# Performance work log

Hardware: AMD Instinct MI355X
Metric: run time of the kernel (lower is better)

## Reference

```python
import jax, jax.numpy as jnp
import numpy as np

B, T, N, F = 8, 24, 207, 16
H = 64            # hidden_dim
DH = 16           # dims_hyper[-1] / node-embedding out
DA = 4 * F        # temporal attention dim_out
DS = 64           # ss_gal gcn out dim (last_ss_gal_dim)
GDEP = 2
ALPHA, BETA, GAMMA = 0.05, 0.95, 0.95
TA = 2.0


def _lin(x, w, b=None):
    y = x @ w
    return y if b is None else y + b


def gcn_hyper(x, A, W, b):
    # x: [B,N,C], A: [N,N] static. h <- a*x + g * einsum('nvc,vw->nwc', h, A)
    h = x
    outs = [h]
    for _ in range(GDEP):
        h = ALPHA * x + GAMMA * jnp.einsum('bvc,vw->bwc', h, A)
        outs.append(h)
    return _lin(jnp.concatenate(outs, axis=-1), W, b)


def gcn_gru(x, A_dyn, A_sta, W, b):
    # x: [B,N,C], A_dyn: [B,N,N], A_sta: [N,N]
    h = x
    outs = [h]
    for _ in range(GDEP):
        h = (ALPHA * x
             + BETA * jnp.einsum('bvw,bvc->bwc', A_dyn, h)     # bmm(A^T, h)
             + GAMMA * jnp.einsum('bvc,vw->bwc', h, A_sta))
        outs.append(h)
    return _lin(jnp.concatenate(outs, axis=-1), W, b)


def gcn_ssgal(x, A, W, b):
    # x: [B*,N,C], A: [B*,N,N]
    h = x
    outs = [h]
    for _ in range(GDEP):
        h = ALPHA * x + GAMMA * jnp.einsum('bvw,bvc->bwc', A, h)
        outs.append(h)
    return _lin(jnp.concatenate(outs, axis=-1), W, b)


def setup_inputs() -> dict:
    key = jax.random.key(0)
    ks = jax.random.split(key, 32)
    i = iter(range(32))
    w = lambda *s: (0.02 * jax.random.normal(ks[next(i)], s, dtype=jnp.float32))
    inp = {
        'input_sequence': jax.random.normal(ks[next(i)], (B, T, N, F), dtype=jnp.float32),
        'static_adj': jax.random.uniform(ks[next(i)], (N, N), dtype=jnp.float32),
        # hyper graph generators: mlp in = (GDEP+1)*H -> DH
        'src_gen_w': w((GDEP + 1) * H, DH), 'src_gen_b': w(DH),
        'tgt_gen_w': w((GDEP + 1) * H, DH), 'tgt_gen_b': w(DH),
        # node embeddings: F -> DH
        'src_emb_w': w(F, DH), 'src_emb_b': w(DH),
        'tgt_emb_w': w(F, DH), 'tgt_emb_b': w(DH),
        # GRU gate GCNs: mlp in = (GDEP+1)*(F+H) -> H
        'gru_z_w': w((GDEP + 1) * (F + H), H), 'gru_z_b': w(H),
        'gru_r_w': w((GDEP + 1) * (F + H), H), 'gru_r_b': w(H),
        'gru_c_w': w((GDEP + 1) * (F + H), H), 'gru_c_b': w(H),
        # temporal attention: F -> DA, score DA -> 1
        'attn_q_w': w(F, DA),
        'attn_k_w': w(F, DA), 'attn_k_b': w(DA),
        'attn_s_w': w(DA, 1),
        # ss_gal spatial gcn: (GDEP+1)*F -> DS
        'sgcn_w': w((GDEP + 1) * F, DS), 'sgcn_b': w(DS),
        # predictors
        'short_w': w(DS, F), 'short_b': w(F),
        'long_w': w(H, F), 'long_b': w(F),
        'fus_w': w(DS + H, F), 'fus_b': w(F),
    }
    return inp


def _forward(input_sequence, static_adj,
             src_gen_w, src_gen_b, tgt_gen_w, tgt_gen_b,
             src_emb_w, src_emb_b, tgt_emb_w, tgt_emb_b,
             gru_z_w, gru_z_b, gru_r_w, gru_r_b, gru_c_w, gru_c_b,
             attn_q_w, attn_k_w, attn_k_b, attn_s_w,
             sgcn_w, sgcn_b,
             short_w, short_b, long_w, long_b, fus_w, fus_b):
    batch, steps, nodes = input_sequence.shape[0], input_sequence.shape[1], input_sequence.shape[2]
    eye = jnp.eye(nodes, dtype=input_sequence.dtype)

    def cell(x_t, h):
        # x_t: [B,N,F], h: [B,N,H]
        src_ctx = gcn_hyper(h, static_adj, src_gen_w, src_gen_b)   # [B,N,DH]
        tgt_ctx = gcn_hyper(h, static_adj, tgt_gen_w, tgt_gen_b)
        s = jnp.tanh(TA * _lin(x_t, src_emb_w, src_emb_b) * src_ctx)
        t = jnp.tanh(TA * _lin(x_t, tgt_emb_w, tgt_emb_b) * tgt_ctx)
        asym = jnp.einsum('bnc,bmc->bnm', s, t) - jnp.einsum('bnc,bmc->bnm', t, s)
        adj = jax.nn.relu(jnp.tanh(TA * asym)) + eye
        adj = adj / (adj.sum(axis=-1, keepdims=True) + 1e-8)
        gi = jnp.concatenate([x_t, h], axis=-1)
        z = jax.nn.sigmoid(gcn_gru(gi, adj, static_adj, gru_z_w, gru_z_b))
        r = jax.nn.sigmoid(gcn_gru(gi, adj, static_adj, gru_r_w, gru_r_b))
        ri = jnp.concatenate([x_t, r * h], axis=-1)
        c = jnp.tanh(gcn_gru(ri, adj, static_adj, gru_c_w, gru_c_b))
        return z * h + (1.0 - z) * c

    h = jnp.zeros((batch, nodes, H), dtype=input_sequence.dtype)
    for t_step in range(0, max(1, steps - 4), 4):
        h = cell(input_sequence[:, t_step], h)

    # ss_gal branch on the last 4 steps
    recent = input_sequence[:, -4:]            # [B,4,N,F]
    target = input_sequence[:, -1]             # [B,N,F]
    # temporal attention
    q = target @ attn_q_w                      # [B,N,DA]
    k = recent @ attn_k_w + attn_k_b           # [B,4,N,DA]
    scores = jnp.tanh(q[:, None, :, None, :] + k[:, :, None, :, :])  # [B,4,N,N,DA]
    scores = jnp.squeeze(scores @ attn_s_w, axis=-1)                  # [B,4,N,N]
    attn = jax.nn.softmax(scores, axis=-1)
    dyn_adj = static_adj[None] + attn.reshape(-1, nodes, nodes)       # [B*4,N,N]
    rh = recent.reshape(-1, nodes, recent.shape[-1])                  # [B*4,N,F]
    rh = gcn_ssgal(rh, dyn_adj, sgcn_w, sgcn_b)                       # [B*4,N,DS]
    rh = jax.nn.relu(rh.reshape(batch, -1, nodes, rh.shape[-1]))      # [B,4,N,DS]
    target = jnp.sum(rh, axis=1)                                       # [B,N,DS]

    short = _lin(target, short_w, short_b)      # [B,N,F]
    h = cell(short, h)                          # final GRU step on short-term prediction
    long = _lin(h, long_w, long_b)              # [B,N,F]
    fused = _lin(jnp.concatenate([target, h], axis=-1), fus_w, fus_b)  # [B,N,F]
    return jnp.stack([short, long, fused], axis=0)  # [3,B,N,F]


def reference(input_sequence, static_adj,
              src_gen_w, src_gen_b, tgt_gen_w, tgt_gen_b,
              src_emb_w, src_emb_b, tgt_emb_w, tgt_emb_b,
              gru_z_w, gru_z_b, gru_r_w, gru_r_b, gru_c_w, gru_c_b,
              attn_q_w, attn_k_w, attn_k_b, attn_s_w,
              sgcn_w, sgcn_b,
              short_w, short_b, long_w, long_b, fus_w, fus_b):
    return _forward(input_sequence, static_adj,
                    src_gen_w, src_gen_b, tgt_gen_w, tgt_gen_b,
                    src_emb_w, src_emb_b, tgt_emb_w, tgt_emb_b,
                    gru_z_w, gru_z_b, gru_r_w, gru_r_b, gru_c_w, gru_c_b,
                    attn_q_w, attn_k_w, attn_k_b, attn_s_w,
                    sgcn_w, sgcn_b,
                    short_w, short_b, long_w, long_b, fus_w, fus_b)
```

## Files before the change

kernel.cpp:

```cpp
#include <hip/hip_runtime.h>


constexpr int B = 8, T = 24, N = 207, F = 16, H = 64, DH = 16;
constexpr int PS = 208;
constexpr float ALPHA = 0.05f, BETA = 0.95f, GAMMA = 0.95f, TA = 2.0f;
constexpr int NF = N * F;
constexpr int BNF = B * N * F;

__device__ __forceinline__ float tanh_fast(float x) { float e = __expf(2.f * x); return 1.f - 2.f / (e + 1.f); }
__device__ __forceinline__ float sigm(float x) { return 1.f / (1.f + __expf(-x)); }
__device__ __forceinline__ float tanh_pade(float x) {
    float x2 = x * x;
    float p = x * (27.f + x2);
    float q = 27.f + 9.f * x2;
    float r = p * __builtin_amdgcn_rcpf(q);
    return fminf(1.f, fmaxf(-1.f, r));
}

__global__ __launch_bounds__(256) void k_build_Ts(const float* __restrict__ adj, float* __restrict__ Ts) {
    int i = blockIdx.x * 256 + threadIdx.x;
    if (i >= N * N) return;
    int w = i / N, v = i % N;
    Ts[(size_t)w * PS + v] = adj[v * N + w];
}

__global__ __launch_bounds__(256) void k_mm_sq(const float* __restrict__ Ain, float* __restrict__ Aout) {
    int bb = blockIdx.z;
    const float* A = Ain + (size_t)bb * PS * PS;
    float* O = Aout + (size_t)bb * PS * PS;
    int w0 = blockIdx.x * 32, v0b = blockIdx.y * 32;
    int tid = threadIdx.x;
    __shared__ float sA[2][32][33], sB[2][32][33];
    float acc[4] = {0, 0, 0, 0};
    int i0 = tid >> 5, j = tid & 31;
    int r = tid >> 3, c4 = (tid & 7) * 4;
    float4 av, bv;
    auto loadT = [&](int u0) {
        av = make_float4(0, 0, 0, 0); bv = make_float4(0, 0, 0, 0);
        int w = w0 + r, u = u0 + r;
        if (w < N) av = *(const float4*)&A[(size_t)w * PS + u0 + c4];
        if (u < N) bv = *(const float4*)&A[(size_t)u * PS + v0b + c4];
    };
    loadT(0);
    int cur = 0;
    for (int t = 0; t < 7; t++) {
        __syncthreads();
        sA[cur][r][c4] = av.x; sA[cur][r][c4 + 1] = av.y; sA[cur][r][c4 + 2] = av.z; sA[cur][r][c4 + 3] = av.w;
        sB[cur][r][c4] = bv.x; sB[cur][r][c4 + 1] = bv.y; sB[cur][r][c4 + 2] = bv.z; sB[cur][r][c4 + 3] = bv.w;
        if (t < 6) loadT((t + 1) * 32);
        __syncthreads();
#pragma unroll 8
        for (int u_ = 0; u_ < 32; u_++) {
            float bvv = sB[cur][u_][j];
#pragma unroll
            for (int k = 0; k < 4; k++) acc[k] += sA[cur][i0 + k * 8][u_] * bvv;
        }
        cur ^= 1;
    }
#pragma unroll
    for (int k = 0; k < 4; k++) {
        int w = w0 + i0 + k * 8, v = v0b + j;
        if (w < N && v < N) O[(size_t)w * PS + v] = acc[k];
    }
}

__global__ __launch_bounds__(256) void k_cell_a(
    const float* __restrict__ h, const float* __restrict__ Ts, const float* __restrict__ A2,
    const float* __restrict__ xseq, int tsel, const float* __restrict__ xbuf,
    const float* __restrict__ Wsrc, const float* __restrict__ bsrc,
    const float* __restrict__ Wtgt, const float* __restrict__ btgt,
    const float* __restrict__ Wes, const float* __restrict__ bes,
    const float* __restrict__ Wet, const float* __restrict__ bet,
    float* __restrict__ s_out, float* __restrict__ t_out, float* __restrict__ catg) {
    int b = blockIdx.y, w0 = blockIdx.x * 16;
    int tid = threadIdx.x, ty = tid >> 4, tx = tid & 15;
    __shared__ float sTs[2][16][33], sA2[2][16][33];
    __shared__ float sH[2][32][64];
    __shared__ float cat[16][193];
    __shared__ float sW[192][16];
    __shared__ float sX[16][16], sWe[16][16];
    float au[4] = {0, 0, 0, 0}, aw[4] = {0, 0, 0, 0};
    const float* hb = h + b * N * H;
    const float* xp = (tsel >= 0) ? (xseq + ((size_t)(b * T + tsel)) * NF) : (xbuf + (size_t)b * NF);
    int pidx = tid & 127;
    int pr = pidx >> 3, pc4 = (pidx & 7) * 4;
    float4 t4;
    float4 h4[2];
    int hr[2], hc[2];
#pragma unroll
    for (int k = 0; k < 2; k++) { int l4 = tid + k * 256; hr[k] = l4 >> 4; hc[k] = (l4 & 15) * 4; }
    auto loadT = [&](int v0) {
        t4 = make_float4(0, 0, 0, 0);
        const float* src = (tid < 128) ? Ts : A2;
        int w = w0 + pr;
        if (w < N) t4 = *(const float4*)&src[(size_t)w * PS + v0 + pc4];
#pragma unroll
        for (int k = 0; k < 2; k++) {
            float4 hv = make_float4(0, 0, 0, 0);
            int v = v0 + hr[k];
            if (v < N) hv = *(const float4*)&hb[(size_t)v * H + hc[k]];
            h4[k] = hv;
        }
    };
    loadT(0);
    int cur = 0;
    for (int t = 0; t < 7; t++) {
        __syncthreads();
        {
            float (*dst)[33] = (tid < 128) ? sTs[cur] : sA2[cur];
            dst[pr][pc4] = t4.x; dst[pr][pc4 + 1] = t4.y; dst[pr][pc4 + 2] = t4.z; dst[pr][pc4 + 3] = t4.w;
        }
#pragma unroll
        for (int k = 0; k < 2; k++) *(float4*)&sH[cur][hr[k]][hc[k]] = h4[k];
        if (t < 6) loadT((t + 1) * 32);
        __syncthreads();
#pragma unroll 8
        for (int v = 0; v < 32; v++) {
            float pu = sTs[cur][ty][v], pw = sA2[cur][ty][v];
#pragma unroll
            for (int j = 0; j < 4; j++) {
                float x = sH[cur][v][tx * 4 + j];
                au[j] += pu * x; aw[j] += pw * x;
            }
        }
        cur ^= 1;
    }
    int w = w0 + ty;
    bool valid = w < N;
    __syncthreads();
    if (valid) {
#pragma unroll
        for (int j = 0; j < 4; j++) {
            int c = tx * 4 + j;
            float hv = hb[w * H + c];
            float u = au[j], w2 = aw[j];
            cat[ty][c] = hv;
            cat[ty][64 + c] = ALPHA * hv + GAMMA * u;
            cat[ty][128 + c] = ALPHA * hv + ALPHA * GAMMA * u + GAMMA * GAMMA * w2;
        }
    } else {
#pragma unroll
        for (int j = 0; j < 4; j++) {
            int c = tx * 4 + j;
            cat[ty][c] = 0; cat[ty][64 + c] = 0; cat[ty][128 + c] = 0;
        }
    }
    {
        float4 wv[3];
#pragma unroll
        for (int k = 0; k < 3; k++) {
            int l4 = tid + k * 256;
            wv[k] = *(const float4*)&Wsrc[l4 * 4];
        }
        float4 xv = make_float4(0, 0, 0, 0), ev = make_float4(0, 0, 0, 0);
        int sr = 0, sc = 0;
        if (tid < 64) {
            sr = tid >> 2; sc = (tid & 3) * 4;
            int n = w0 + sr;
            if (n < N) xv = *(const float4*)&xp[(size_t)n * F + sc];
            ev = *(const float4*)&Wes[tid * 4];
        }
#pragma unroll
        for (int k = 0; k < 3; k++) {
            int l4 = tid + k * 256;
            int r = l4 >> 2, c4 = (l4 & 3) * 4;
            *(float4*)&sW[r][c4] = wv[k];
        }
        if (tid < 64) {
            *(float4*)&sX[sr][sc] = xv;
            *(float4*)&sWe[sr][sc] = ev;
        }
    }
    __syncthreads();
    if (valid) {
#pragma unroll
        for (int j = 0; j < 5; j++) {
            int c = tx * 5 + j;
            float v = (c < 16) ? sX[ty][c] : hb[w * H + (c - 16)];
            catg[((size_t)(b * N + w)) * 240 + c] = v;
        }
    }
    {
        float ctx = bsrc[tx];
#pragma unroll 8
        for (int c = 0; c < 192; c++) ctx += cat[ty][c] * sW[c][tx];
        float xe = bes[tx];
#pragma unroll
        for (int f = 0; f < 16; f++) xe += sX[ty][f] * sWe[f][tx];
        if (valid) s_out[(b * N + w) * DH + tx] = tanh_fast(TA * xe * ctx);
    }
    __syncthreads();
    {
        float4 wv[3];
#pragma unroll
        for (int k = 0; k < 3; k++) {
            int l4 = tid + k * 256;
            wv[k] = *(const float4*)&Wtgt[l4 * 4];
        }
        float4 ev = make_float4(0, 0, 0, 0);
        if (tid < 64) ev = *(const float4*)&Wet[tid * 4];
#pragma unroll
        for (int k = 0; k < 3; k++) {
            int l4 = tid + k * 256;
            int r = l4 >> 2, c4 = (l4 & 3) * 4;
            *(float4*)&sW[r][c4] = wv[k];
        }
        if (tid < 64) *(float4*)&sWe[tid >> 2][(tid & 3) * 4] = ev;
    }
    __syncthreads();
    {
        float ctx = btgt[tx];
#pragma unroll 8
        for (int c = 0; c < 192; c++) ctx += cat[ty][c] * sW[c][tx];
        float xe = bet[tx];
#pragma unroll
        for (int f = 0; f < 16; f++) xe += sX[ty][f] * sWe[f][tx];
        if (valid) t_out[(b * N + w) * DH + tx] = tanh_fast(TA * xe * ctx);
    }
}

__global__ __launch_bounds__(256) void k_cell_bP(const float* __restrict__ s_in, const float* __restrict__ t_in,
                                                 const float* __restrict__ adj, float* __restrict__ P) {
    int b = blockIdx.y, v0 = blockIdx.x * 16;
    int tid = threadIdx.x, ty = tid >> 4, tx = tid & 15;
    __shared__ float sS[N][17], sT[N][17];
    for (int l4 = tid; l4 < 828; l4 += 256) {
        float4 sv = *(const float4*)&s_in[(size_t)b * N * 16 + l4 * 4];
        float4 tv = *(const float4*)&t_in[(size_t)b * N * 16 + l4 * 4];
        int r = l4 >> 2, c = (l4 & 3) * 4;
        sS[r][c] = sv.x; sS[r][c + 1] = sv.y; sS[r][c + 2] = sv.z; sS[r][c + 3] = sv.w;
        sT[r][c] = tv.x; sT[r][c + 1] = tv.y; sT[r][c + 2] = tv.z; sT[r][c + 3] = tv.w;
    }
    __syncthreads();
    int v = v0 + ty;
    bool valid = v < N;
    int vc = valid ? v : (N - 1);
    float sv[16], tv[16];
#pragma unroll
    for (int k = 0; k < 16; k++) { sv[k] = sS[vc][k]; tv[k] = sT[vc][k]; }
    float val[13];
    float rsum = 0.f;
#pragma unroll
    for (int idx = 0; idx < 13; idx++) {
        int w = tx + 16 * idx;
        float r = 0.f;
        if (w < N) {
            float a = 0.f;
#pragma unroll
            for (int k = 0; k < 16; k++) a += sv[k] * sT[w][k] - tv[k] * sS[w][k];
            r = tanh_fast(TA * a);
            r = r > 0.f ? r : 0.f;
            if (w == v) r += 1.f;
        }
        val[idx] = r;
        rsum += r;
    }
    float tot = rsum;
    for (int d = 8; d > 0; d >>= 1) tot += __shfl_down(tot, d, 16);
    tot = __shfl(tot, 0, 16);
    float rinv = BETA / (tot + 1e-8f);
    if (valid) {
        float* Pb = P + (size_t)b * PS * PS;
#pragma unroll
        for (int idx = 0; idx < 13; idx++) {
            int w = tx + 16 * idx;
            if (w < N) Pb[(size_t)w * PS + v] = val[idx] * rinv + GAMMA * adj[v * N + w];
        }
    }
}

__global__ __launch_bounds__(256) void k_combineT(const float* __restrict__ Ain, const float* __restrict__ rs,
                                                  const float* __restrict__ Ts, float* __restrict__ Pout,
                                                  float cA, float cT) {
    int bt = blockIdx.z;
    int w0 = blockIdx.x * 32, v0 = blockIdx.y * 32;
    int tid = threadIdx.x;
    __shared__ float tile[32][33];
    __shared__ float rsv[32];
    int r = tid >> 3, c4 = (tid & 7) * 4;
    float4 a4 = make_float4(0, 0, 0, 0);
    int v = v0 + r;
    if (v < N) a4 = *(const float4*)&Ain[(size_t)bt * PS * PS + (size_t)v * PS + w0 + c4];
    tile[r][c4] = a4.x; tile[r][c4 + 1] = a4.y; tile[r][c4 + 2] = a4.z; tile[r][c4 + 3] = a4.w;
    if (tid < 32) {
        int vv = v0 + tid;
        rsv[tid] = (vv < N) ? (cA / rs[bt * N + vv]) : 0.f;
    }
    __syncthreads();
    for (int l = tid; l < 1024; l += 256) {
        int i = l >> 5, j = l & 31;
        int w = w0 + i, vv = v0 + j;
        if (w < N && vv < N)
            Pout[(size_t)bt * PS * PS + (size_t)w * PS + vv] = tile[j][i] * rsv[j] + cT * Ts[(size_t)w * PS + vv];
    }
}

__global__ __launch_bounds__(256) void k_prop2(const float* __restrict__ P, const float* __restrict__ P2,
                                               float* __restrict__ cat) {
    int b = blockIdx.y, w0 = blockIdx.x * 16, c0 = blockIdx.z * 16;
    int tid = threadIdx.x, ty = tid >> 4, tx = tid & 15;
    const float* Pb = P + (size_t)b * PS * PS;
    const float* P2b = P2 + (size_t)b * PS * PS;
    __shared__ float sP[2][16][33], sP2[2][16][33], sX[2][32][17];
    float a1 = 0.f, a2 = 0.f;
    int pr = tid >> 4, pc = (tid & 15) * 2;
    int xr = tid >> 3, xc = (tid & 7) * 2;
    float2 pv, p2v, xv;
    auto loadT = [&](int v0) {
        pv = make_float2(0, 0); p2v = make_float2(0, 0); xv = make_float2(0, 0);
        int w = w0 + pr;
        if (w < N) {
            pv = *(const float2*)&Pb[(size_t)w * PS + v0 + pc];
            p2v = *(const float2*)&P2b[(size_t)w * PS + v0 + pc];
        }
        int vv = v0 + xr;
        if (vv < N) xv = *(const float2*)&cat[((size_t)(b * N + vv)) * 240 + c0 + xc];
    };
    loadT(0);
    int cur = 0;
    for (int t = 0; t < 7; t++) {
        __syncthreads();
        sP[cur][pr][pc] = pv.x; sP[cur][pr][pc + 1] = pv.y;
        sP2[cur][pr][pc] = p2v.x; sP2[cur][pr][pc + 1] = p2v.y;
        sX[cur][xr][xc] = xv.x; sX[cur][xr][xc + 1] = xv.y;
        if (t < 6) loadT((t + 1) * 32);
        __syncthreads();
#pragma unroll 8
        for (int v_ = 0; v_ < 32; v_++) {
            float xx = sX[cur][v_][tx];
            a1 += sP[cur][ty][v_] * xx;
            a2 += sP2[cur][ty][v_] * xx;
        }
        cur ^= 1;
    }
    int w = w0 + ty, c = c0 + tx;
    if (w < N) {
        size_t base = ((size_t)(b * N + w)) * 240;
        float x0 = cat[base + c];
        cat[base + 80 + c] = ALPHA * x0 + a1;
        cat[base + 160 + c] = ALPHA * x0 + ALPHA * a1 + a2;
    }
}

__global__ __launch_bounds__(256) void k_gate(
    const float* __restrict__ cat,
    const float* __restrict__ Wa, const float* __restrict__ ba,
    const float* __restrict__ Wb, const float* __restrict__ bb,
    int baseMode,
    const float* __restrict__ xseq, int tsel, const float* __restrict__ xbuf,
    float* __restrict__ zbuf, float* __restrict__ ricat,
    float* __restrict__ h,
    const float* __restrict__ target,
    const float* __restrict__ Wlong, const float* __restrict__ blong,
    const float* __restrict__ Wfus, const float* __restrict__ bfus,
    float* __restrict__ out) {
    int mode = baseMode + blockIdx.z;
    const float* W = (mode == 1) ? Wb : Wa;
    const float* bias = (mode == 1) ? bb : ba;
    int b = blockIdx.y, w0 = blockIdx.x * 16;
    int tid = threadIdx.x, ty = tid >> 4, tx = tid & 15;
    __shared__ float sC[16][241];
    __shared__ float sW[2][48][65];
    __shared__ float hrow[16][65], trow[16][65];
    for (int l4 = tid; l4 < 960; l4 += 256) {
        int r = l4 / 60, cc = (l4 % 60) * 4;
        int w = w0 + r;
        float4 v4 = make_float4(0, 0, 0, 0);
        if (w < N) v4 = *(const float4*)&cat[((size_t)(b * N + w)) * 240 + cc];
        sC[r][cc] = v4.x; sC[r][cc + 1] = v4.y; sC[r][cc + 2] = v4.z; sC[r][cc + 3] = v4.w;
    }
    float acc[4];
#pragma unroll
    for (int j = 0; j < 4; j++) acc[j] = bias[tx * 4 + j];
    float4 wv[3];
#pragma unroll
    for (int k = 0; k < 3; k++) wv[k] = *(const float4*)&W[(tid + k * 256) * 4];
    int cur = 0;
    for (int ch = 0; ch < 5; ch++) {
        __syncthreads();
#pragma unroll
        for (int k = 0; k < 3; k++) {
            int l4 = tid + k * 256;
            int r = l4 >> 4, cc = (l4 & 15) * 4;
            sW[cur][r][cc] = wv[k].x; sW[cur][r][cc + 1] = wv[k].y; sW[cur][r][cc + 2] = wv[k].z; sW[cur][r][cc + 3] = wv[k].w;
        }
        if (ch < 4) {
#pragma unroll
            for (int k = 0; k < 3; k++) wv[k] = *(const float4*)&W[(size_t)(ch + 1) * 48 * 64 + (tid + k * 256) * 4];
        }
        __syncthreads();
        int c0 = ch * 48;
#pragma unroll 8
        for (int cc = 0; cc < 48; cc++) {
            float cv = sC[ty][c0 + cc];
#pragma unroll
            for (int j = 0; j < 4; j++) acc[j] += cv * sW[cur][cc][tx * 4 + j];
        }
        cur ^= 1;
    }
    int w = w0 + ty;
    bool valid = w < N;
    if (mode == 0) {
        if (valid) {
#pragma unroll
            for (int j = 0; j < 4; j++) zbuf[((size_t)(b * N + w)) * 64 + tx * 4 + j] = sigm(acc[j]);
        }
    } else if (mode == 1) {
        if (valid) {
#pragma unroll
            for (int j = 0; j < 4; j++) {
                int o = tx * 4 + j;
                ricat[((size_t)(b * N + w)) * 240 + 16 + o] = sigm(acc[j]) * h[((size_t)(b * N + w)) * 64 + o];
            }
            if (tx < 4) {
                const float* xp = (tsel >= 0) ? (xseq + ((size_t)(b * T + tsel)) * NF) : (xbuf + (size_t)b * NF);
#pragma unroll
                for (int j = 0; j < 4; j++) {
                    int c = tx * 4 + j;
                    ricat[((size_t)(b * N + w)) * 240 + c] = xp[w * F + c];
                }
            }
        }
    } else {
#pragma unroll
        for (int j = 0; j < 4; j++) {
            int o = tx * 4 + j;
            float cval = tanh_fast(acc[j]);
            float zv = 0.f, hv = 0.f;
            if (valid) { zv = zbuf[((size_t)(b * N + w)) * 64 + o]; hv = h[((size_t)(b * N + w)) * 64 + o]; }
            float hn = zv * hv + (1.f - zv) * cval;
            if (valid) h[((size_t)(b * N + w)) * 64 + o] = hn;
            hrow[ty][o] = valid ? hn : 0.f;
        }
        if (mode == 3) {
            for (int l = tid; l < 1024; l += 256) {
                int i = l >> 6, o = l & 63;
                int ww = w0 + i;
                trow[i][o] = (ww < N) ? target[((size_t)(b * N + ww)) * 64 + o] : 0.f;
            }
            __syncthreads();
            float lg = blong[tx];
            float fs = bfus[tx];
            for (int o = 0; o < 64; o++) {
                lg += hrow[ty][o] * Wlong[o * 16 + tx];
                fs += trow[ty][o] * Wfus[o * 16 + tx] + hrow[ty][o] * Wfus[(64 + o) * 16 + tx];
            }
            if (valid) {
                out[((size_t)1 * B * N + b * N + w) * 16 + tx] = lg;
                out[((size_t)2 * B * N + b * N + w) * 16 + tx] = fs;
            }
        }
    }
}

__global__ __launch_bounds__(256) void k_attn2(const float* __restrict__ inp,
                                               const float* __restrict__ Wq, const float* __restrict__ Wk,
                                               const float* __restrict__ kb, const float* __restrict__ sw_,
                                               float* __restrict__ attnU, float* __restrict__ rsum) {
    int bt = blockIdx.z, b = bt >> 2, tau = bt & 3;
    int n0 = blockIdx.x * 16, m0 = blockIdx.y * 16;
    int tid = threadIdx.x, ti = tid >> 4, tj = tid & 15;
    __shared__ float sQ[16][65], sK[16][65];
    __shared__ float sWq[16][64], sWk[16][64];
    __shared__ float sXq[16][16], sXk[16][16];
    __shared__ float ssw[64], skb[64];
    const float* xq = inp + ((size_t)(b * T + (T - 1))) * NF;
    const float* xk = inp + ((size_t)(b * T + 20 + tau)) * NF;
    {
        float4 wq4 = *(const float4*)&Wq[tid * 4];
        float4 wk4 = *(const float4*)&Wk[tid * 4];
        *(float4*)&sWq[tid >> 4][(tid & 15) * 4] = wq4;
        *(float4*)&sWk[tid >> 4][(tid & 15) * 4] = wk4;
        if (tid < 64) { ssw[tid] = sw_[tid]; skb[tid] = kb[tid]; }
        if (tid >= 64 && tid < 128) {
            int idx = tid - 64;
            int r = idx >> 2, c4 = (idx & 3) * 4;
            int n = n0 + r, m = m0 + r;
            float4 a = make_float4(0, 0, 0, 0), c = make_float4(0, 0, 0, 0);
            if (n < N) a = *(const float4*)&xq[(size_t)n * F + c4];
            if (m < N) c = *(const float4*)&xk[(size_t)m * F + c4];
            *(float4*)&sXq[r][c4] = a;
            *(float4*)&sXk[r][c4] = c;
        }
    }
    __syncthreads();
    {
#pragma unroll
        for (int j = 0; j < 4; j++) {
            int o = tj * 4 + j;
            float aq = 0.f, ak = skb[o];
#pragma unroll
            for (int f = 0; f < 16; f++) { aq += sXq[ti][f] * sWq[f][o]; ak += sXk[ti][f] * sWk[f][o]; }
            sQ[ti][o] = aq; sK[ti][o] = ak;
        }
    }
    __syncthreads();
    float sc = 0.f;
#pragma unroll 4
    for (int d = 0; d < 64; d++) sc += tanh_pade(sQ[ti][d] + sK[tj][d]) * ssw[d];
    int n = n0 + ti, m = m0 + tj;
    bool vn = n < N, vm = m < N;
    float e = (vn && vm) ? __expf(sc) : 0.f;
    float part = e;
    for (int d = 8; d > 0; d >>= 1) part += __shfl_down(part, d, 16);
    if (tj == 0 && vn) atomicAdd(&rsum[bt * N + n], part);
    if (vn && vm) attnU[(size_t)bt * PS * PS + (size_t)n * PS + m] = e;
}

__global__ __launch_bounds__(256) void k_prop_xr(const float* __restrict__ Pd, const float* __restrict__ inp,
                                                 float* __restrict__ x1) {
    int bt = blockIdx.y, w0 = blockIdx.x * 16;
    int b = bt >> 2, tau = bt & 3;
    const float* xb = inp + ((size_t)(b * T + 20 + tau)) * NF;
    const float* Pb = Pd + (size_t)bt * PS * PS;
    int tid = threadIdx.x, ty = tid >> 4, tx = tid & 15;
    __shared__ float sP[2][16][33];
    __shared__ float sX[2][32][17];
    float acc = 0.f;
    int prr = tid >> 3, pcc = (tid & 7) * 4;
    int xrr = (tid - 128) >> 2, xcc = ((tid - 128) & 3) * 4;
    float4 pv, xv;
    auto loadT = [&](int v0) {
        pv = make_float4(0, 0, 0, 0); xv = make_float4(0, 0, 0, 0);
        if (tid < 128) {
            int w = w0 + prr;
            if (w < N) pv = *(const float4*)&Pb[(size_t)w * PS + v0 + pcc];
        } else {
            int v = v0 + xrr;
            if (v < N) xv = *(const float4*)&xb[(size_t)v * F + xcc];
        }
    };
    loadT(0);
    int cur = 0;
    for (int t = 0; t < 7; t++) {
        __syncthreads();
        if (tid < 128) {
            sP[cur][prr][pcc] = pv.x; sP[cur][prr][pcc + 1] = pv.y; sP[cur][prr][pcc + 2] = pv.z; sP[cur][prr][pcc + 3] = pv.w;
        } else {
            sX[cur][xrr][xcc] = xv.x; sX[cur][xrr][xcc + 1] = xv.y; sX[cur][xrr][xcc + 2] = xv.z; sX[cur][xrr][xcc + 3] = xv.w;
        }
        if (t < 6) loadT((t + 1) * 32);
        __syncthreads();
#pragma unroll 8
        for (int v = 0; v < 32; v++) acc += sP[cur][ty][v] * sX[cur][v][tx];
        cur ^= 1;
    }
    int w = w0 + ty;
    if (w < N) x1[((size_t)(bt * N + w)) * 16 + tx] = ALPHA * xb[w * F + tx] + acc;
}

__global__ __launch_bounds__(256) void k_sgc2(const float* __restrict__ Pd, const float* __restrict__ x1,
                                              const float* __restrict__ inp,
                                              const float* __restrict__ Ws, const float* __restrict__ bs,
                                              float* __restrict__ target) {
    int bt = blockIdx.y, b = bt >> 2, tau = bt & 3, w0 = blockIdx.x * 16;
    const float* xb = inp + ((size_t)(b * T + 20 + tau)) * NF;
    const float* Pb = Pd + (size_t)bt * PS * PS;
    int tid = threadIdx.x, ty = tid >> 4, tx = tid & 15;
    __shared__ float sP[2][16][33], sX[2][32][17], cat[16][48], sW[48][64];
    float acc = 0.f;
    int prr = tid >> 3, pcc = (tid & 7) * 4;
    int xrr = (tid - 128) >> 2, xcc = ((tid - 128) & 3) * 4;
    float4 pv, xv;
    auto loadT = [&](int v0) {
        pv = make_float4(0, 0, 0, 0); xv = make_float4(0, 0, 0, 0);
        if (tid < 128) {
            int w = w0 + prr;
            if (w < N) pv = *(const float4*)&Pb[(size_t)w * PS + v0 + pcc];
        } else {
            int v = v0 + xrr;
            if (v < N) xv = *(const float4*)&x1[((size_t)(bt * N + v)) * 16 + xcc];
        }
    };
    loadT(0);
    int cur = 0;
    for (int t = 0; t < 7; t++) {
        __syncthreads();
        if (tid < 128) {
            sP[cur][prr][pcc] = pv.x; sP[cur][prr][pcc + 1] = pv.y; sP[cur][prr][pcc + 2] = pv.z; sP[cur][prr][pcc + 3] = pv.w;
        } else {
            sX[cur][xrr][xcc] = xv.x; sX[cur][xrr][xcc + 1] = xv.y; sX[cur][xrr][xcc + 2] = xv.z; sX[cur][xrr][xcc + 3] = xv.w;
        }
        if (t < 6) loadT((t + 1) * 32);
        __syncthreads();
#pragma unroll 8
        for (int v = 0; v < 32; v++) acc += sP[cur][ty][v] * sX[cur][v][tx];
        cur ^= 1;
    }
    int w = w0 + ty;
    bool valid = w < N;
    __syncthreads();
    for (int l = tid; l < 512; l += 256) {
        int i = l >> 5, c = l & 31;
        int ww = w0 + i;
        float vv = 0;
        if (ww < N) {
            if (c < 16) vv = xb[ww * F + c];
            else vv = x1[((size_t)bt * N + ww) * 16 + (c - 16)];
        }
        cat[i][c] = vv;
    }
    {
        float x0 = valid ? xb[w * F + tx] : 0.f;
        cat[ty][32 + tx] = ALPHA * x0 + acc;
    }
    {
        float4 wv[3];
#pragma unroll
        for (int k = 0; k < 3; k++) wv[k] = *(const float4*)&Ws[(tid + k * 256) * 4];
#pragma unroll
        for (int k = 0; k < 3; k++) {
            int l4 = tid + k * 256;
            *(float4*)&sW[l4 >> 4][(l4 & 15) * 4] = wv[k];
        }
    }
    __syncthreads();
    float a[4];
#pragma unroll
    for (int j = 0; j < 4; j++) a[j] = bs[tx * 4 + j];
#pragma unroll 8
    for (int cc = 0; cc < 48; cc++) {
        float cv = cat[ty][cc];
#pragma unroll
        for (int j = 0; j < 4; j++) a[j] += cv * sW[cc][tx * 4 + j];
    }
    if (valid) {
#pragma unroll
        for (int j = 0; j < 4; j++) {
            float r = a[j] > 0.f ? a[j] : 0.f;
            atomicAdd(&target[(b * N + w) * 64 + tx * 4 + j], r);
        }
    }
}

__global__ __launch_bounds__(256) void k_short(const float* __restrict__ target,
                                               const float* __restrict__ Wsh, const float* __restrict__ bsh,
                                               float* __restrict__ out, float* __restrict__ xshort) {
    int b = blockIdx.y, n0 = blockIdx.x * 16;
    int tid = threadIdx.x, ty = tid >> 4, tx = tid & 15;
    __shared__ float trow[16][65], sW[64][16];
    {
        int r = tid >> 4, c4 = (tid & 15) * 4;
        int n = n0 + r;
        float4 tv = make_float4(0, 0, 0, 0);
        if (n < N) tv = *(const float4*)&target[((size_t)(b * N + n)) * 64 + c4];
        trow[r][c4] = tv.x; trow[r][c4 + 1] = tv.y; trow[r][c4 + 2] = tv.z; trow[r][c4 + 3] = tv.w;
        float4 wv = *(const float4*)&Wsh[tid * 4];
        *(float4*)&sW[tid >> 2][(tid & 3) * 4] = wv;
    }
    __syncthreads();
    float a = bsh[tx];
#pragma unroll 8
    for (int o = 0; o < 64; o++) a += trow[ty][o] * sW[o][tx];
    int n = n0 + ty;
    if (n < N) {
        out[((size_t)0 * B * N + b * N + n) * 16 + tx] = a;
        xshort[(b * N + n) * 16 + tx] = a;
    }
}

extern "C" void kernel_launch(void* const* d_in, const int* in_sizes, int n_in,
                              void* d_out, int out_size, void* d_ws, size_t ws_size,
                              hipStream_t stream) {
    const float* inp = (const float*)d_in[0];
    const float* adj = (const float*)d_in[1];
    const float* src_gen_w = (const float*)d_in[2];
    const float* src_gen_b = (const float*)d_in[3];
    const float* tgt_gen_w = (const float*)d_in[4];
    const float* tgt_gen_b = (const float*)d_in[5];
    const float* src_emb_w = (const float*)d_in[6];
    const float* src_emb_b = (const float*)d_in[7];
    const float* tgt_emb_w = (const float*)d_in[8];
    const float* tgt_emb_b = (const float*)d_in[9];
    const float* gru_z_w = (const float*)d_in[10];
    const float* gru_z_b = (const float*)d_in[11];
    const float* gru_r_w = (const float*)d_in[12];
    const float* gru_r_b = (const float*)d_in[13];
    const float* gru_c_w = (const float*)d_in[14];
    const float* gru_c_b = (const float*)d_in[15];
    const float* attn_q_w = (const float*)d_in[16];
    const float* attn_k_w = (const float*)d_in[17];
    const float* attn_k_b = (const float*)d_in[18];
    const float* attn_s_w = (const float*)d_in[19];
    const float* sgcn_w = (const float*)d_in[20];
    const float* sgcn_b = (const float*)d_in[21];
    const float* short_w = (const float*)d_in[22];
    const float* short_b = (const float*)d_in[23];
    const float* long_w = (const float*)d_in[24];
    const float* long_b = (const float*)d_in[25];
    const float* fus_w = (const float*)d_in[26];
    const float* fus_b = (const float*)d_in[27];
    float* out = (float*)d_out;

    float* ws = (float*)d_ws;
    size_t off = 0;
    auto A = [&](size_t n) { n = (n + 3) & ~(size_t)3; float* p = ws + off; off += n; return p; };
    float* Ts = A((size_t)PS * PS);
    float* A2 = A((size_t)PS * PS);
    float* h = A((size_t)B * N * H);
    float* sbuf = A((size_t)B * N * DH);
    float* tbuf = A((size_t)B * N * DH);
    float* P = A((size_t)B * PS * PS);
    float* P2 = A((size_t)B * PS * PS);
    float* catg = A((size_t)B * N * 240);
    float* catc = A((size_t)B * N * 240);
    float* zb = A((size_t)B * N * 64);
    float* attnU = A((size_t)32 * PS * PS);
    float* Pd = A((size_t)32 * PS * PS);
    float* x1 = A((size_t)32 * NF);
    float* target = A((size_t)B * N * 64);
    float* rsum = A((size_t)32 * N);
    float* xshort = A(BNF);
    (void)ws_size; (void)in_sizes; (void)n_in; (void)out_size;

    hipMemsetAsync(h, 0, sizeof(float) * B * N * H, stream);
    hipMemsetAsync(target, 0, sizeof(float) * (B * N * 64), stream);
    hipMemsetAsync(rsum, 0, sizeof(float) * (32 * N), stream);
    k_build_Ts<<<(N * N + 255) / 256, 256, 0, stream>>>(adj, Ts);
    k_mm_sq<<<dim3(7, 7, 1), 256, 0, stream>>>(Ts, A2);

    auto run_cell = [&](int tsel, const float* xbuf, int finalFlag) {
        k_cell_a<<<dim3(13, B), 256, 0, stream>>>(h, Ts, A2, inp, tsel, xbuf,
                                                  src_gen_w, src_gen_b, tgt_gen_w, tgt_gen_b,
                                                  src_emb_w, src_emb_b, tgt_emb_w, tgt_emb_b, sbuf, tbuf, catg);
        k_cell_bP<<<dim3(13, B), 256, 0, stream>>>(sbuf, tbuf, adj, P);
        k_mm_sq<<<dim3(7, 7, B), 256, 0, stream>>>(P, P2);
        k_prop2<<<dim3(13, B, 5), 256, 0, stream>>>(P, P2, catg);
        k_gate<<<dim3(13, B, 2), 256, 0, stream>>>(catg, gru_z_w, gru_z_b, gru_r_w, gru_r_b, 0,
                                                   inp, tsel, xbuf, zb, catc, h,
                                                   nullptr, nullptr, nullptr, nullptr, nullptr, nullptr);
        k_prop2<<<dim3(13, B, 5), 256, 0, stream>>>(P, P2, catc);
        k_gate<<<dim3(13, B, 1), 256, 0, stream>>>(catc, gru_c_w, gru_c_b, nullptr, nullptr, 2 + finalFlag,
                                                   nullptr, 0, nullptr, zb, nullptr, h,
                                                   target, long_w, long_b, fus_w, fus_b, out);
    };

    for (int t = 0; t < 20; t += 4) run_cell(t, nullptr, 0);

    k_attn2<<<dim3(13, 13, 32), 256, 0, stream>>>(inp, attn_q_w, attn_k_w, attn_k_b, attn_s_w, attnU, rsum);
    k_combineT<<<dim3(7, 7, 32), 256, 0, stream>>>(attnU, rsum, Ts, Pd, GAMMA, GAMMA);
    k_prop_xr<<<dim3(13, 32), 256, 0, stream>>>(Pd, inp, x1);
    k_sgc2<<<dim3(13, 32), 256, 0, stream>>>(Pd, x1, inp, sgcn_w, sgcn_b, target);
    k_short<<<dim3(13, B), 256, 0, stream>>>(target, short_w, short_b, out, xshort);

    run_cell(-1, xshort, 1);
}
```

Measured before the change: 702.2 us.

## Replace per-step P² matmul with sequential propagation and retile attention scores

Each GRU cell no longer forms P² with a 207x207x207 batched matmul. It now runs one propagation hop in k_prop1, and the gate kernel performs the second hop P·h1 itself before the gate GEMM. The temporal-attention kernel now computes a 2x2 output block per thread over 32x32 tiles. It also drops the tanh clamp on the Padé approximation, which can push tanh_pnc(x) past ±1 for large |x|. The aim is to cut the O(N³) work and P2 traffic per cell, at the cost of recomputing hop 2 inside both the z/r and c gate blocks and removing sP2 double buffering.

Result: faster. 661.6 us (-5.8%).

```diff
diff --git a/kernel.cpp b/kernel.cpp
--- a/kernel.cpp
+++ b/kernel.cpp
@@ -9,12 +9,11 @@
 
 __device__ __forceinline__ float tanh_fast(float x) { float e = __expf(2.f * x); return 1.f - 2.f / (e + 1.f); }
 __device__ __forceinline__ float sigm(float x) { return 1.f / (1.f + __expf(-x)); }
-__device__ __forceinline__ float tanh_pade(float x) {
+__device__ __forceinline__ float tanh_pnc(float x) {
     float x2 = x * x;
     float p = x * (27.f + x2);
     float q = 27.f + 9.f * x2;
-    float r = p * __builtin_amdgcn_rcpf(q);
-    return fminf(1.f, fmaxf(-1.f, r));
+    return p * __builtin_amdgcn_rcpf(q);
 }
 
 __global__ __launch_bounds__(256) void k_build_Ts(const float* __restrict__ adj, float* __restrict__ Ts) {
@@ -25,9 +24,8 @@
 }
 
 __global__ __launch_bounds__(256) void k_mm_sq(const float* __restrict__ Ain, float* __restrict__ Aout) {
-    int bb = blockIdx.z;
-    const float* A = Ain + (size_t)bb * PS * PS;
-    float* O = Aout + (size_t)bb * PS * PS;
+    const float* A = Ain;
+    float* O = Aout;
     int w0 = blockIdx.x * 32, v0b = blockIdx.y * 32;
     int tid = threadIdx.x;
     __shared__ float sA[2][32][33], sB[2][32][33];
@@ -295,24 +293,19 @@
     }
 }
 
-__global__ __launch_bounds__(256) void k_prop2(const float* __restrict__ P, const float* __restrict__ P2,
-                                               float* __restrict__ cat) {
+__global__ __launch_bounds__(256) void k_prop1(const float* __restrict__ P, float* __restrict__ cat) {
     int b = blockIdx.y, w0 = blockIdx.x * 16, c0 = blockIdx.z * 16;
     int tid = threadIdx.x, ty = tid >> 4, tx = tid & 15;
     const float* Pb = P + (size_t)b * PS * PS;
-    const float* P2b = P2 + (size_t)b * PS * PS;
-    __shared__ float sP[2][16][33], sP2[2][16][33], sX[2][32][17];
-    float a1 = 0.f, a2 = 0.f;
+    __shared__ float sP[2][16][33], sX[2][32][17];
+    float a1 = 0.f;
     int pr = tid >> 4, pc = (tid & 15) * 2;
     int xr = tid >> 3, xc = (tid & 7) * 2;
-    float2 pv, p2v, xv;
+    float2 pv, xv;
     auto loadT = [&](int v0) {
-        pv = make_float2(0, 0); p2v = make_float2(0, 0); xv = make_float2(0, 0);
+        pv = make_float2(0, 0); xv = make_float2(0, 0);
         int w = w0 + pr;
-        if (w < N) {
-            pv = *(const float2*)&Pb[(size_t)w * PS + v0 + pc];
-            p2v = *(const float2*)&P2b[(size_t)w * PS + v0 + pc];
-        }
+        if (w < N) pv = *(const float2*)&Pb[(size_t)w * PS + v0 + pc];
         int vv = v0 + xr;
         if (vv < N) xv = *(const float2*)&cat[((size_t)(b * N + vv)) * 240 + c0 + xc];
     };
@@ -321,29 +314,22 @@
     for (int t = 0; t < 7; t++) {
         __syncthreads();
         sP[cur][pr][pc] = pv.x; sP[cur][pr][pc + 1] = pv.y;
-        sP2[cur][pr][pc] = p2v.x; sP2[cur][pr][pc + 1] = p2v.y;
         sX[cur][xr][xc] = xv.x; sX[cur][xr][xc + 1] = xv.y;
         if (t < 6) loadT((t + 1) * 32);
         __syncthreads();
 #pragma unroll 8
-        for (int v_ = 0; v_ < 32; v_++) {
-            float xx = sX[cur][v_][tx];
-            a1 += sP[cur][ty][v_] * xx;
-            a2 += sP2[cur][ty][v_] * xx;
-        }
+        for (int v_ = 0; v_ < 32; v_++) a1 += sP[cur][ty][v_] * sX[cur][v_][tx];
         cur ^= 1;
     }
     int w = w0 + ty, c = c0 + tx;
     if (w < N) {
         size_t base = ((size_t)(b * N + w)) * 240;
-        float x0 = cat[base + c];
-        cat[base + 80 + c] = ALPHA * x0 + a1;
-        cat[base + 160 + c] = ALPHA * x0 + ALPHA * a1 + a2;
+        cat[base + 80 + c] = ALPHA * cat[base + c] + a1;
     }
 }
 
 __global__ __launch_bounds__(256) void k_gate(
-    const float* __restrict__ cat,
+    const float* __restrict__ cat, const float* __restrict__ P,
     const float* __restrict__ Wa, const float* __restrict__ ba,
     const float* __restrict__ Wb, const float* __restrict__ bb,
     int baseMode,
@@ -359,30 +345,70 @@
     const float* bias = (mode == 1) ? bb : ba;
     int b = blockIdx.y, w0 = blockIdx.x * 16;
     int tid = threadIdx.x, ty = tid >> 4, tx = tid & 15;
+    const float* Pb = P + (size_t)b * PS * PS;
     __shared__ float sC[16][241];
-    __shared__ float sW[2][48][65];
+    __shared__ float sP[16][33];
+    __shared__ float sX[32][81];
+    __shared__ float sW[48][65];
     __shared__ float hrow[16][65], trow[16][65];
-    for (int l4 = tid; l4 < 960; l4 += 256) {
-        int r = l4 / 60, cc = (l4 % 60) * 4;
+    for (int l4 = tid; l4 < 640; l4 += 256) {
+        int r = l4 / 40, c4 = (l4 % 40) * 4;
         int w = w0 + r;
         float4 v4 = make_float4(0, 0, 0, 0);
-        if (w < N) v4 = *(const float4*)&cat[((size_t)(b * N + w)) * 240 + cc];
-        sC[r][cc] = v4.x; sC[r][cc + 1] = v4.y; sC[r][cc + 2] = v4.z; sC[r][cc + 3] = v4.w;
-    }
-    float acc[4];
-#pragma unroll
-    for (int j = 0; j < 4; j++) acc[j] = bias[tx * 4 + j];
+        if (w < N) v4 = *(const float4*)&cat[((size_t)(b * N + w)) * 240 + c4];
+        sC[r][c4] = v4.x; sC[r][c4 + 1] = v4.y; sC[r][c4 + 2] = v4.z; sC[r][c4 + 3] = v4.w;
+    }
+    float acc[5] = {0, 0, 0, 0, 0};
+    int prr = tid >> 4, prc = (tid & 15) * 2;
+    int xrow = tid & 31, xc0 = (tid >> 5) * 10;
+    float2 pv;
+    float2 xv[5];
+    auto loadT = [&](int v0) {
+        pv = make_float2(0, 0);
+        int w = w0 + prr;
+        if (w < N) pv = *(const float2*)&Pb[(size_t)w * PS + v0 + prc];
+        int v = v0 + xrow;
+#pragma unroll
+        for (int k = 0; k < 5; k++) xv[k] = make_float2(0, 0);
+        if (v < N) {
+            const float* src = &cat[((size_t)(b * N + v)) * 240 + 80 + xc0];
+#pragma unroll
+            for (int k = 0; k < 5; k++) xv[k] = *(const float2*)&src[k * 2];
+        }
+    };
+    loadT(0);
+    for (int t = 0; t < 7; t++) {
+        __syncthreads();
+        sP[prr][prc] = pv.x; sP[prr][prc + 1] = pv.y;
+#pragma unroll
+        for (int k = 0; k < 5; k++) { sX[xrow][xc0 + 2 * k] = xv[k].x; sX[xrow][xc0 + 2 * k + 1] = xv[k].y; }
+        if (t < 6) loadT((t + 1) * 32);
+        __syncthreads();
+#pragma unroll 8
+        for (int v = 0; v < 32; v++) {
+            float p = sP[ty][v];
+#pragma unroll
+            for (int j = 0; j < 5; j++) acc[j] += p * sX[v][tx * 5 + j];
+        }
+    }
+#pragma unroll
+    for (int j = 0; j < 5; j++) {
+        int c = tx * 5 + j;
+        sC[ty][160 + c] = ALPHA * sC[ty][c] + acc[j];
+    }
     float4 wv[3];
 #pragma unroll
     for (int k = 0; k < 3; k++) wv[k] = *(const float4*)&W[(tid + k * 256) * 4];
-    int cur = 0;
+    float ga[4];
+#pragma unroll
+    for (int j = 0; j < 4; j++) ga[j] = bias[tx * 4 + j];
     for (int ch = 0; ch < 5; ch++) {
         __syncthreads();
 #pragma unroll
         for (int k = 0; k < 3; k++) {
             int l4 = tid + k * 256;
             int r = l4 >> 4, cc = (l4 & 15) * 4;
-            sW[cur][r][cc] = wv[k].x; sW[cur][r][cc + 1] = wv[k].y; sW[cur][r][cc + 2] = wv[k].z; sW[cur][r][cc + 3] = wv[k].w;
+            sW[r][cc] = wv[k].x; sW[r][cc + 1] = wv[k].y; sW[r][cc + 2] = wv[k].z; sW[r][cc + 3] = wv[k].w;
         }
         if (ch < 4) {
 #pragma unroll
@@ -394,23 +420,22 @@
         for (int cc = 0; cc < 48; cc++) {
             float cv = sC[ty][c0 + cc];
 #pragma unroll
-            for (int j = 0; j < 4; j++) acc[j] += cv * sW[cur][cc][tx * 4 + j];
-        }
-        cur ^= 1;
+            for (int j = 0; j < 4; j++) ga[j] += cv * sW[cc][tx * 4 + j];
+        }
     }
     int w = w0 + ty;
     bool valid = w < N;
     if (mode == 0) {
         if (valid) {
 #pragma unroll
-            for (int j = 0; j < 4; j++) zbuf[((size_t)(b * N + w)) * 64 + tx * 4 + j] = sigm(acc[j]);
+            for (int j = 0; j < 4; j++) zbuf[((size_t)(b * N + w)) * 64 + tx * 4 + j] = sigm(ga[j]);
         }
     } else if (mode == 1) {
         if (valid) {
 #pragma unroll
             for (int j = 0; j < 4; j++) {
                 int o = tx * 4 + j;
-                ricat[((size_t)(b * N + w)) * 240 + 16 + o] = sigm(acc[j]) * h[((size_t)(b * N + w)) * 64 + o];
+                ricat[((size_t)(b * N + w)) * 240 + 16 + o] = sigm(ga[j]) * h[((size_t)(b * N + w)) * 64 + o];
             }
             if (tx < 4) {
                 const float* xp = (tsel >= 0) ? (xseq + ((size_t)(b * T + tsel)) * NF) : (xbuf + (size_t)b * NF);
@@ -425,7 +450,7 @@
 #pragma unroll
         for (int j = 0; j < 4; j++) {
             int o = tx * 4 + j;
-            float cval = tanh_fast(acc[j]);
+            float cval = tanh_fast(ga[j]);
             float zv = 0.f, hv = 0.f;
             if (valid) { zv = zbuf[((size_t)(b * N + w)) * 64 + o]; hv = h[((size_t)(b * N + w)) * 64 + o]; }
             float hn = zv * hv + (1.f - zv) * cval;
@@ -458,11 +483,11 @@
                                                const float* __restrict__ kb, const float* __restrict__ sw_,
                                                float* __restrict__ attnU, float* __restrict__ rsum) {
     int bt = blockIdx.z, b = bt >> 2, tau = bt & 3;
-    int n0 = blockIdx.x * 16, m0 = blockIdx.y * 16;
+    int n0 = blockIdx.x * 32, m0 = blockIdx.y * 32;
     int tid = threadIdx.x, ti = tid >> 4, tj = tid & 15;
-    __shared__ float sQ[16][65], sK[16][65];
+    __shared__ float sQ[32][65], sK[32][65];
     __shared__ float sWq[16][64], sWk[16][64];
-    __shared__ float sXq[16][16], sXk[16][16];
+    __shared__ float sXq[32][17], sXk[32][17];
     __shared__ float ssw[64], skb[64];
     const float* xq = inp + ((size_t)(b * T + (T - 1))) * NF;
     const float* xk = inp + ((size_t)(b * T + 20 + tau)) * NF;
@@ -472,39 +497,67 @@
         *(float4*)&sWq[tid >> 4][(tid & 15) * 4] = wq4;
         *(float4*)&sWk[tid >> 4][(tid & 15) * 4] = wk4;
         if (tid < 64) { ssw[tid] = sw_[tid]; skb[tid] = kb[tid]; }
-        if (tid >= 64 && tid < 128) {
-            int idx = tid - 64;
-            int r = idx >> 2, c4 = (idx & 3) * 4;
-            int n = n0 + r, m = m0 + r;
-            float4 a = make_float4(0, 0, 0, 0), c = make_float4(0, 0, 0, 0);
+        int idx = tid & 127;
+        int r = idx >> 2, c4 = (idx & 3) * 4;
+        if (tid < 128) {
+            float4 a = make_float4(0, 0, 0, 0);
+            int n = n0 + r;
             if (n < N) a = *(const float4*)&xq[(size_t)n * F + c4];
+            sXq[r][c4] = a.x; sXq[r][c4 + 1] = a.y; sXq[r][c4 + 2] = a.z; sXq[r][c4 + 3] = a.w;
+        } else {
+            float4 c = make_float4(0, 0, 0, 0);
+            int m = m0 + r;
             if (m < N) c = *(const float4*)&xk[(size_t)m * F + c4];
-            *(float4*)&sXq[r][c4] = a;
-            *(float4*)&sXk[r][c4] = c;
-        }
-    }
-    __syncthreads();
-    {
-#pragma unroll
-        for (int j = 0; j < 4; j++) {
-            int o = tj * 4 + j;
+            sXk[r][c4] = c.x; sXk[r][c4 + 1] = c.y; sXk[r][c4 + 2] = c.z; sXk[r][c4 + 3] = c.w;
+        }
+    }
+    __syncthreads();
+    {
+        int r = tid >> 3, o0 = (tid & 7) * 8;
+        float xr[16], xkr[16];
+#pragma unroll
+        for (int f = 0; f < 16; f++) { xr[f] = sXq[r][f]; xkr[f] = sXk[r][f]; }
+#pragma unroll
+        for (int j = 0; j < 8; j++) {
+            int o = o0 + j;
             float aq = 0.f, ak = skb[o];
 #pragma unroll
-            for (int f = 0; f < 16; f++) { aq += sXq[ti][f] * sWq[f][o]; ak += sXk[ti][f] * sWk[f][o]; }
-            sQ[ti][o] = aq; sK[ti][o] = ak;
-        }
-    }
-    __syncthreads();
-    float sc = 0.f;
-#pragma unroll 4
-    for (int d = 0; d < 64; d++) sc += tanh_pade(sQ[ti][d] + sK[tj][d]) * ssw[d];
-    int n = n0 + ti, m = m0 + tj;
-    bool vn = n < N, vm = m < N;
-    float e = (vn && vm) ? __expf(sc) : 0.f;
-    float part = e;
-    for (int d = 8; d > 0; d >>= 1) part += __shfl_down(part, d, 16);
-    if (tj == 0 && vn) atomicAdd(&rsum[bt * N + n], part);
-    if (vn && vm) attnU[(size_t)bt * PS * PS + (size_t)n * PS + m] = e;
+            for (int f = 0; f < 16; f++) { aq += xr[f] * sWq[f][o]; ak += xkr[f] * sWk[f][o]; }
+            sQ[r][o] = aq; sK[r][o] = ak;
+        }
+    }
+    __syncthreads();
+    float s00 = 0.f, s01 = 0.f, s10 = 0.f, s11 = 0.f;
+#pragma unroll 2
+    for (int d = 0; d < 64; d++) {
+        float w = ssw[d];
+        float q1 = sQ[ti][d], q2 = sQ[ti + 16][d];
+        float k1 = sK[tj][d], k2 = sK[tj + 16][d];
+        s00 += tanh_pnc(q1 + k1) * w;
+        s01 += tanh_pnc(q1 + k2) * w;
+        s10 += tanh_pnc(q2 + k1) * w;
+        s11 += tanh_pnc(q2 + k2) * w;
+    }
+    int n1 = n0 + ti, n2 = n0 + ti + 16, m1 = m0 + tj, m2 = m0 + tj + 16;
+    bool vn1 = n1 < N, vn2 = n2 < N, vm1 = m1 < N, vm2 = m2 < N;
+    float e00 = (vn1 && vm1) ? __expf(s00) : 0.f;
+    float e01 = (vn1 && vm2) ? __expf(s01) : 0.f;
+    float e10 = (vn2 && vm1) ? __expf(s10) : 0.f;
+    float e11 = (vn2 && vm2) ? __expf(s11) : 0.f;
+    float part1 = e00 + e01, part2 = e10 + e11;
+    for (int d = 8; d > 0; d >>= 1) {
+        part1 += __shfl_down(part1, d, 16);
+        part2 += __shfl_down(part2, d, 16);
+    }
+    if (tj == 0) {
+        if (vn1) atomicAdd(&rsum[bt * N + n1], part1);
+        if (vn2) atomicAdd(&rsum[bt * N + n2], part2);
+    }
+    size_t base = (size_t)bt * PS * PS;
+    if (vn1 && vm1) attnU[base + (size_t)n1 * PS + m1] = e00;
+    if (vn1 && vm2) attnU[base + (size_t)n1 * PS + m2] = e01;
+    if (vn2 && vm1) attnU[base + (size_t)n2 * PS + m1] = e10;
+    if (vn2 && vm2) attnU[base + (size_t)n2 * PS + m2] = e11;
 }
 
 __global__ __launch_bounds__(256) void k_prop_xr(const float* __restrict__ Pd, const float* __restrict__ inp,
@@ -701,7 +754,6 @@
     float* sbuf = A((size_t)B * N * DH);
     float* tbuf = A((size_t)B * N * DH);
     float* P = A((size_t)B * PS * PS);
-    float* P2 = A((size_t)B * PS * PS);
     float* catg = A((size_t)B * N * 240);
     float* catc = A((size_t)B * N * 240);
     float* zb = A((size_t)B * N * 64);
@@ -717,27 +769,26 @@
     hipMemsetAsync(target, 0, sizeof(float) * (B * N * 64), stream);
     hipMemsetAsync(rsum, 0, sizeof(float) * (32 * N), stream);
     k_build_Ts<<<(N * N + 255) / 256, 256, 0, stream>>>(adj, Ts);
-    k_mm_sq<<<dim3(7, 7, 1), 256, 0, stream>>>(Ts, A2);
+    k_mm_sq<<<dim3(7, 7), 256, 0, stream>>>(Ts, A2);
 
     auto run_cell = [&](int tsel, const float* xbuf, int finalFlag) {
         k_cell_a<<<dim3(13, B), 256, 0, stream>>>(h, Ts, A2, inp, tsel, xbuf,
                                                   src_gen_w, src_gen_b, tgt_gen_w, tgt_gen_b,
                                                   src_emb_w, src_emb_b, tgt_emb_w, tgt_emb_b, sbuf, tbuf, catg);
         k_cell_bP<<<dim3(13, B), 256, 0, stream>>>(sbuf, tbuf, adj, P);
-        k_mm_sq<<<dim3(7, 7, B), 256, 0, stream>>>(P, P2);
-        k_prop2<<<dim3(13, B, 5), 256, 0, stream>>>(P, P2, catg);
-        k_gate<<<dim3(13, B, 2), 256, 0, stream>>>(catg, gru_z_w, gru_z_b, gru_r_w, gru_r_b, 0,
+        k_prop1<<<dim3(13, B, 5), 256, 0, stream>>>(P, catg);
+        k_gate<<<dim3(13, B, 2), 256, 0, stream>>>(catg, P, gru_z_w, gru_z_b, gru_r_w, gru_r_b, 0,
                                                    inp, tsel, xbuf, zb, catc, h,
                                                    nullptr, nullptr, nullptr, nullptr, nullptr, nullptr);
-        k_prop2<<<dim3(13, B, 5), 256, 0, stream>>>(P, P2, catc);
-        k_gate<<<dim3(13, B, 1), 256, 0, stream>>>(catc, gru_c_w, gru_c_b, nullptr, nullptr, 2 + finalFlag,
+        k_prop1<<<dim3(13, B, 5), 256, 0, stream>>>(P, catc);
+        k_gate<<<dim3(13, B, 1), 256, 0, stream>>>(catc, P, gru_c_w, gru_c_b, nullptr, nullptr, 2 + finalFlag,
                                                    nullptr, 0, nullptr, zb, nullptr, h,
                                                    target, long_w, long_b, fus_w, fus_b, out);
     };
 
     for (int t = 0; t < 20; t += 4) run_cell(t, nullptr, 0);
 
-    k_attn2<<<dim3(13, 13, 32), 256, 0, stream>>>(inp, attn_q_w, attn_k_w, attn_k_b, attn_s_w, attnU, rsum);
+    k_attn2<<<dim3(7, 7, 32), 256, 0, stream>>>(inp, attn_q_w, attn_k_w, attn_k_b, attn_s_w, attnU, rsum);
     k_combineT<<<dim3(7, 7, 32), 256, 0, stream>>>(attnU, rsum, Ts, Pd, GAMMA, GAMMA);
     k_prop_xr<<<dim3(13, 32), 256, 0, stream>>>(Pd, inp, x1);
     k_sgc2<<<dim3(13, 32), 256, 0, stream>>>(Pd, x1, inp, sgcn_w, sgcn_b, target);
```
